# Kernel tuning notes

Hardware: AMD Instinct MI355X
Metric: run time of the kernel (lower is better)

## Reference

```python
import jax, jax.numpy as jnp
import numpy as np

B, L, D, H = 1, 4096, 512, 8
HD = D // H  # head_dim = 64


def _relative_bias(rel, length):
    # rel: [H, 2L] learnable; returns [H, L, L] relative position bias
    h = rel.shape[0]
    r = jnp.tile(rel, (1, length))                      # [H, 2L*L]
    r = r[:, : length * (2 * length - 1)]
    r = r.reshape(h, length, 2 * length - 1)
    return r[..., length - 1:]                          # [H, L, L]


def setup_inputs() -> dict:
    key = jax.random.key(0)
    ks = jax.random.split(key, 12)
    std = D ** -0.5
    inp = {
        "x": jax.random.normal(ks[0], (B, L, D), jnp.float32),
        "pos_embed": jax.random.normal(ks[1], (L, D), jnp.float32) * std,
        "rel_bias": jnp.zeros((H, 2 * L), jnp.float32) + 0.01 * jax.random.normal(ks[2], (H, 2 * L), jnp.float32),
        "Wq": jax.random.normal(ks[3], (D, H, HD), jnp.float32) * std,
        "bq": jnp.zeros((H, HD), jnp.float32),
        "Wk": jax.random.normal(ks[4], (D, H, HD), jnp.float32) * std,
        "bk": jnp.zeros((H, HD), jnp.float32),
        "Wv": jax.random.normal(ks[5], (D, H, HD), jnp.float32) * std,
        "bv": jnp.zeros((H, HD), jnp.float32),
        "Wo": jax.random.normal(ks[6], (H, HD, D), jnp.float32) * (D ** -0.5),
        "bo": jnp.zeros((D,), jnp.float32),
    }
    return inp


def reference(x, pos_embed, rel_bias, Wq, bq, Wk, bk, Wv, bv, Wo, bo):
    # Positional embedding
    x = x + pos_embed
    # QKV projections: [B, L, H, HD]
    q = jnp.einsum("bld,dhk->blhk", x, Wq) + bq
    k = jnp.einsum("bld,dhk->blhk", x, Wk) + bk
    v = jnp.einsum("bld,dhk->blhk", x, Wv) + bv
    # Scaled dot-product attention with relative attention bias
    depth = q.shape[-1]
    q = q / jnp.sqrt(jnp.asarray(depth, q.dtype))
    scores = jnp.einsum("bqhd,bkhd->bhqk", q, k)       # [B, H, L, L]
    bias = _relative_bias(rel_bias, x.shape[1])         # [H, L, L]
    scores = scores + bias[None]
    attn = jax.nn.softmax(scores, axis=-1)
    out = jnp.einsum("bhqk,bkhd->bqhd", attn, v)       # [B, L, H, HD]
    # Output projection back to D
    return jnp.einsum("bqhd,hdD->bqD", out, Wo) + bo
```

## Files before the change

### kernel.cpp

```cpp
#include <hip/hip_runtime.h>
#include <hip/hip_bf16.h>


typedef __attribute__((ext_vector_type(8))) short bf16x8;
typedef __attribute__((ext_vector_type(4))) short bf16x4;
typedef __attribute__((ext_vector_type(4))) float f32x4;
typedef __attribute__((ext_vector_type(2))) unsigned u32x2;

#define QSCALE (0.125f * 1.4426950408889634f)

__device__ __forceinline__ short f2bf(float f) {
    unsigned u = __builtin_bit_cast(unsigned, f);
    u += 0x7fff + ((u >> 16) & 1);
    return (short)(u >> 16);
}

__device__ __forceinline__ f32x4 mfma32(bf16x8 a, bf16x8 b, f32x4 c) {
    return __builtin_amdgcn_mfma_f32_16x16x32_bf16(a, b, c, 0, 0, 0);
}

__device__ __forceinline__ unsigned cvtpk(float a, float b) {
    unsigned r;
    asm("v_cvt_pk_bf16_f32 %0, %1, %2" : "=v"(r) : "v"(a), "v"(b));
    return r;
}

__global__ __launch_bounds__(256) void k_prep_xp(const float* __restrict__ x,
                                                 const float* __restrict__ pos,
                                                 short* __restrict__ xp) {
    int i = (blockIdx.x * 256 + threadIdx.x) * 8;
    float4 a0 = *(const float4*)(x + i);
    float4 a1 = *(const float4*)(x + i + 4);
    float4 b0 = *(const float4*)(pos + i);
    float4 b1 = *(const float4*)(pos + i + 4);
    bf16x8 v;
    v[0] = f2bf(a0.x + b0.x); v[1] = f2bf(a0.y + b0.y);
    v[2] = f2bf(a0.z + b0.z); v[3] = f2bf(a0.w + b0.w);
    v[4] = f2bf(a1.x + b1.x); v[5] = f2bf(a1.y + b1.y);
    v[6] = f2bf(a1.z + b1.z); v[7] = f2bf(a1.w + b1.w);
    *(bf16x8*)(xp + i) = v;
}

__global__ __launch_bounds__(256) void k_prep_wqkv(const float* __restrict__ Wq,
                                                   const float* __restrict__ Wk,
                                                   const float* __restrict__ Wv,
                                                   short* __restrict__ WT) {
    int idx = blockIdx.x * 256 + threadIdx.x;
    int n = idx >> 9, k = idx & 511;
    int nn = n & 511;
    const float* src = (n < 512) ? Wq : (n < 1024 ? Wk : Wv);
    float scale = (n < 512) ? QSCALE : 1.0f;
    WT[idx] = f2bf(src[k * 512 + nn] * scale);
}

__global__ __launch_bounds__(256) void k_prep_wo(const float* __restrict__ Wo,
                                                 short* __restrict__ WoT) {
    int idx = blockIdx.x * 256 + threadIdx.x;
    int n = idx >> 9, k = idx & 511;
    WoT[idx] = f2bf(Wo[k * 512 + n]);
}

__global__ __launch_bounds__(256) void k_prep_rel2(const float* __restrict__ rel,
                                                   float* __restrict__ rel2) {
    int i = blockIdx.x * 256 + threadIdx.x;
    rel2[i] = rel[i] * 1.4426950408889634f;
}

__global__ __launch_bounds__(256) void k_vt(const short* __restrict__ Vg,
                                            short* __restrict__ VT) {
    __shared__ short tile[64][72];
    const int tid = threadIdx.x;
    const int h = blockIdx.y, kvb = blockIdx.x * 64;
    const short* src = Vg + (size_t)h * 4096 * 64;
    short* dst = VT + (size_t)h * 64 * 4096;
    #pragma unroll
    for (int i = 0; i < 2; ++i) {
        int ch = tid + 256 * i;
        int r = ch >> 3, c = (ch & 7) * 8;
        *(uint4*)&tile[r][c] = *(const uint4*)(src + (size_t)(kvb + r) * 64 + c);
    }
    __syncthreads();
    #pragma unroll
    for (int i = 0; i < 2; ++i) {
        int ch = tid + 256 * i;
        int d = ch >> 3, kc = (ch & 7) * 8;
        bf16x8 v;
        #pragma unroll
        for (int j = 0; j < 8; ++j) v[j] = tile[kc + j][d];
        *(bf16x8*)(dst + (size_t)d * 4096 + kvb + kc) = v;
    }
}

template <int MODE>
__global__ __launch_bounds__(256) void k_gemm(const short* __restrict__ A,
                                              const short* __restrict__ Bt,
                                              const float* __restrict__ bias0,
                                              const float* __restrict__ bias1,
                                              const float* __restrict__ bias2,
                                              short* __restrict__ Qg,
                                              short* __restrict__ Kg,
                                              short* __restrict__ Vg,
                                              float* __restrict__ Cout) {
    __shared__ short Al[128][72];
    __shared__ short Bl[128][72];
    const int tid = threadIdx.x;
    const int lane = tid & 63, wid = tid >> 6;
    const int wm = wid >> 1, wn = wid & 1;
    const int mb = blockIdx.y * 128, nb = blockIdx.x * 128;
    const int lr = lane & 15, lg = lane >> 4;

    f32x4 acc[4][4] = {};

    for (int kk = 0; kk < 512; kk += 64) {
        #pragma unroll
        for (int i = 0; i < 4; ++i) {
            int o = tid + 256 * i;
            int row = o >> 3, c8 = (o & 7) * 8;
            *(uint4*)(&Al[row][c8]) = *(const uint4*)(A + (size_t)(mb + row) * 512 + kk + c8);
            *(uint4*)(&Bl[row][c8]) = *(const uint4*)(Bt + (size_t)(nb + row) * 512 + kk + c8);
        }
        __syncthreads();
        #pragma unroll
        for (int ks = 0; ks < 2; ++ks) {
            bf16x8 af[4], bfr[4];
            #pragma unroll
            for (int t = 0; t < 4; ++t) {
                af[t]  = *(const bf16x8*)(&Al[wm * 64 + t * 16 + lr][ks * 32 + lg * 8]);
                bfr[t] = *(const bf16x8*)(&Bl[wn * 64 + t * 16 + lr][ks * 32 + lg * 8]);
            }
            #pragma unroll
            for (int mt = 0; mt < 4; ++mt)
                #pragma unroll
                for (int nt = 0; nt < 4; ++nt)
                    acc[mt][nt] = mfma32(af[mt], bfr[nt], acc[mt][nt]);
        }
        __syncthreads();
    }

    #pragma unroll
    for (int mt = 0; mt < 4; ++mt) {
        #pragma unroll
        for (int nt = 0; nt < 4; ++nt) {
            #pragma unroll
            for (int r = 0; r < 4; ++r) {
                int m = mb + wm * 64 + mt * 16 + lg * 4 + r;
                int n = nb + wn * 64 + nt * 16 + lr;
                float v = acc[mt][nt][r];
                if (MODE == 0) {
                    int which = n >> 9;
                    int nn = n & 511;
                    int hh = nn >> 6, hd = nn & 63;
                    const float* bp = (which == 0) ? bias0 : (which == 1 ? bias1 : bias2);
                    v += bp[nn] * (which == 0 ? QSCALE : 1.0f);
                    short* dst = (which == 0) ? Qg : (which == 1 ? Kg : Vg);
                    dst[((size_t)hh * 4096 + m) * 64 + hd] = f2bf(v);
                } else {
                    Cout[(size_t)m * 512 + n] = v + bias0[n];
                }
            }
        }
    }
}

__global__ __launch_bounds__(256, 2) void k_attn3(const short* __restrict__ Qg,
                                                  const short* __restrict__ Kg,
                                                  const short* __restrict__ VT,
                                                  const float* __restrict__ rel2,
                                                  short* __restrict__ AO) {
    __shared__ __align__(16) char smem[70656];

    const int tid = threadIdx.x;
    const int lane = tid & 63, sp = tid >> 6;
    const int lr = lane & 15, lg = lane >> 4;
    const int bid = blockIdx.x;
    const int h = bid & 7;
    const int qb = (bid >> 3) * 64;

    short* Pw = (short*)smem + sp * 1152;

    const short* Qh = Qg + (size_t)h * 4096 * 64;
    const short* Kh = Kg + (size_t)h * 4096 * 64;
    const short* VTh = VT + (size_t)h * 64 * 4096;

    bf16x8 qf[4][2];
    #pragma unroll
    for (int qt = 0; qt < 4; ++qt)
        #pragma unroll
        for (int dk = 0; dk < 2; ++dk)
            qf[qt][dk] = *(const bf16x8*)(Qh + (size_t)(qb + qt * 16 + lr) * 64 + dk * 32 + lg * 8);

    const int kvbase = sp * 1024;
    const short* kp = Kh + (size_t)kvbase * 64;
    const short* vp = VTh + kvbase;
    const float* bp = rel2 + h * 8192 + (kvbase + 4095 - qb) + lg * 4 - lr;

    f32x4 acc[4][4] = {};
    f32x4 lacc[4] = {};

    bf16x8 ones;
    #pragma unroll
    for (int i = 0; i < 8; ++i) ones[i] = (short)0x3F80;

    #pragma unroll 1
    for (int it = 0; it < 16; ++it) {
        bf16x8 kf[4][2];
        #pragma unroll
        for (int t = 0; t < 4; ++t) {
            kf[t][0] = *(const bf16x8*)(kp + (size_t)(t * 16 + lr) * 64 + lg * 8);
            kf[t][1] = *(const bf16x8*)(kp + (size_t)(t * 16 + lr) * 64 + 32 + lg * 8);
        }
        bf16x8 vf[4][2];
        #pragma unroll
        for (int dt = 0; dt < 4; ++dt)
            #pragma unroll
            for (int w = 0; w < 2; ++w)
                vf[dt][w] = *(const bf16x8*)(vp + (size_t)(dt * 16 + lr) * 4096 + w * 32 + lg * 8);

        #pragma unroll
        for (int qt = 0; qt < 4; ++qt) {
            f32x4 cin[4];
            #pragma unroll
            for (int t = 0; t < 4; ++t)
                #pragma unroll
                for (int r = 0; r < 4; ++r)
                    cin[t][r] = bp[(t - qt) * 16 + r];

            unsigned pk0[4], pk1[4];
            #pragma unroll
            for (int t = 0; t < 4; ++t) {
                f32x4 z = mfma32(kf[t][0], qf[qt][0], cin[t]);
                z = mfma32(kf[t][1], qf[qt][1], z);
                float p0 = exp2f(z[0]), p1 = exp2f(z[1]);
                float p2 = exp2f(z[2]), p3 = exp2f(z[3]);
                pk0[t] = cvtpk(p0, p1);
                pk1[t] = cvtpk(p2, p3);
            }

            asm volatile("s_waitcnt lgkmcnt(0)" ::: "memory");
            __builtin_amdgcn_sched_barrier(0);
            #pragma unroll
            for (int t = 0; t < 4; ++t) {
                u32x2 pk;
                pk[0] = pk0[t]; pk[1] = pk1[t];
                *(u32x2*)(Pw + lr * 72 + t * 16 + lg * 4) = pk;
            }
            __builtin_amdgcn_sched_barrier(0);

            bf16x8 pb0 = *(const bf16x8*)(Pw + lr * 72 + lg * 8);
            bf16x8 pb1 = *(const bf16x8*)(Pw + lr * 72 + 32 + lg * 8);

            lacc[qt] = mfma32(ones, pb0, lacc[qt]);
            lacc[qt] = mfma32(ones, pb1, lacc[qt]);

            #pragma unroll
            for (int dt = 0; dt < 4; ++dt) {
                acc[qt][dt] = mfma32(vf[dt][0], pb0, acc[qt][dt]);
                acc[qt][dt] = mfma32(vf[dt][1], pb1, acc[qt][dt]);
            }
        }
        kp += 64 * 64;
        vp += 64;
        bp += 64;
    }

    __builtin_amdgcn_sched_barrier(0);
    __syncthreads();
    __builtin_amdgcn_sched_barrier(0);

    float* Opart = (float*)smem;
    float* Lpart = (float*)(smem + 69632);
    #pragma unroll
    for (int qt = 0; qt < 4; ++qt) {
        #pragma unroll
        for (int dt = 0; dt < 4; ++dt)
            *(f32x4*)&Opart[((sp * 4 + qt) * 16 + lr) * 68 + dt * 16 + lg * 4] = acc[qt][dt];
        if (lg == 0) Lpart[(sp * 4 + qt) * 16 + lr] = lacc[qt][0];
    }
    __builtin_amdgcn_sched_barrier(0);
    __syncthreads();
    __builtin_amdgcn_sched_barrier(0);
    {
        const int qi = tid >> 2, quad = tid & 3;
        const int qt2 = qi >> 4, qr = qi & 15;
        f32x4 s0 = {}, s1 = {}, s2 = {}, s3 = {};
        float lt = 0.f;
        #pragma unroll
        for (int s = 0; s < 4; ++s) {
            const float* o = &Opart[((s * 4 + qt2) * 16 + qr) * 68 + quad * 16];
            s0 += *(const f32x4*)(o + 0);
            s1 += *(const f32x4*)(o + 4);
            s2 += *(const f32x4*)(o + 8);
            s3 += *(const f32x4*)(o + 12);
            lt += Lpart[(s * 4 + qt2) * 16 + qr];
        }
        float inv = 1.0f / lt;
        bf16x8 o0, o1;
        o0[0] = f2bf(s0[0] * inv); o0[1] = f2bf(s0[1] * inv);
        o0[2] = f2bf(s0[2] * inv); o0[3] = f2bf(s0[3] * inv);
        o0[4] = f2bf(s1[0] * inv); o0[5] = f2bf(s1[1] * inv);
        o0[6] = f2bf(s1[2] * inv); o0[7] = f2bf(s1[3] * inv);
        o1[0] = f2bf(s2[0] * inv); o1[1] = f2bf(s2[1] * inv);
        o1[2] = f2bf(s2[2] * inv); o1[3] = f2bf(s2[3] * inv);
        o1[4] = f2bf(s3[0] * inv); o1[5] = f2bf(s3[1] * inv);
        o1[6] = f2bf(s3[2] * inv); o1[7] = f2bf(s3[3] * inv);
        short* dst = AO + (size_t)(qb + qi) * 512 + h * 64 + quad * 16;
        *(bf16x8*)(dst) = o0;
        *(bf16x8*)(dst + 8) = o1;
    }
}

extern "C" void kernel_launch(void* const* d_in, const int* in_sizes, int n_in,
                              void* d_out, int out_size, void* d_ws, size_t ws_size,
                              hipStream_t stream) {
    const float* x   = (const float*)d_in[0];
    const float* pos = (const float*)d_in[1];
    const float* rel = (const float*)d_in[2];
    const float* Wq  = (const float*)d_in[3];
    const float* bq  = (const float*)d_in[4];
    const float* Wk  = (const float*)d_in[5];
    const float* bk  = (const float*)d_in[6];
    const float* Wv  = (const float*)d_in[7];
    const float* bv  = (const float*)d_in[8];
    const float* Wo  = (const float*)d_in[9];
    const float* bo  = (const float*)d_in[10];
    float* out = (float*)d_out;

    char* ws = (char*)d_ws;
    short* xp    = (short*)ws;  ws += (size_t)4096 * 512 * 2;
    short* WqkvT = (short*)ws;  ws += (size_t)1536 * 512 * 2;
    short* WoT   = (short*)ws;  ws += (size_t)512 * 512 * 2;
    short* Qg    = (short*)ws;  ws += (size_t)8 * 4096 * 64 * 2;
    short* Kg    = (short*)ws;  ws += (size_t)8 * 4096 * 64 * 2;
    short* Vg    = (short*)ws;  ws += (size_t)8 * 4096 * 64 * 2;
    short* AO    = (short*)ws;  ws += (size_t)4096 * 512 * 2;
    float* rel2  = (float*)ws;  ws += (size_t)8 * 8192 * 4;
    short* VT    = xp;

    k_prep_xp<<<dim3(4096 * 512 / (256 * 8)), 256, 0, stream>>>(x, pos, xp);
    k_prep_wqkv<<<dim3(1536 * 512 / 256), 256, 0, stream>>>(Wq, Wk, Wv, WqkvT);
    k_prep_wo<<<dim3(512 * 512 / 256), 256, 0, stream>>>(Wo, WoT);
    k_prep_rel2<<<dim3(8 * 8192 / 256), 256, 0, stream>>>(rel, rel2);

    k_gemm<0><<<dim3(12, 32), 256, 0, stream>>>(xp, WqkvT, bq, bk, bv, Qg, Kg, Vg, nullptr);
    k_vt<<<dim3(64, 8), 256, 0, stream>>>(Vg, VT);
    k_attn3<<<dim3(512), 256, 0, stream>>>(Qg, Kg, VT, rel2, AO);
    k_gemm<1><<<dim3(4, 32), 256, 0, stream>>>(AO, WoT, bo, nullptr, nullptr,
                                               nullptr, nullptr, nullptr, out);
}
```

Before: 130.0 us.

## Split attention KV range across blocks and merge partials in separate kernel

The attention kernel changes from one block per 64 queries, with four waves splitting the KV range and reducing in shared memory, to blocks whose four waves each own 32 queries of a 128-query tile while the block handles one quarter of the KV range. Partial outputs and row sums go to global workspace, and a new merge kernel sums the four partials, normalises and writes bf16. The aim is to cut LDS use and registers so four blocks fit per CU, doubling the grid for occupancy. The cost is extra global traffic for fp32 partials (about 32MB written and read) plus another kernel launch.

After: 330.1 us. +153.9%, slower.

```diff
diff --git a/kernel.cpp b/kernel.cpp
--- a/kernel.cpp
+++ b/kernel.cpp
@@ -162,40 +162,42 @@
     }
 }
 
-__global__ __launch_bounds__(256, 2) void k_attn3(const short* __restrict__ Qg,
+__global__ __launch_bounds__(256, 4) void k_attn4(const short* __restrict__ Qg,
                                                   const short* __restrict__ Kg,
                                                   const short* __restrict__ VT,
                                                   const float* __restrict__ rel2,
-                                                  short* __restrict__ AO) {
-    __shared__ __align__(16) char smem[70656];
+                                                  float* __restrict__ Opar,
+                                                  float* __restrict__ Lpar) {
+    __shared__ __align__(16) char smem[9216];
 
     const int tid = threadIdx.x;
-    const int lane = tid & 63, sp = tid >> 6;
+    const int lane = tid & 63, wv = tid >> 6;
     const int lr = lane & 15, lg = lane >> 4;
     const int bid = blockIdx.x;
     const int h = bid & 7;
-    const int qb = (bid >> 3) * 64;
-
-    short* Pw = (short*)smem + sp * 1152;
+    const int s = (bid >> 3) & 3;
+    const int qb = (bid >> 5) * 128 + wv * 32;
+
+    short* Pw = (short*)smem + wv * 1152;
 
     const short* Qh = Qg + (size_t)h * 4096 * 64;
     const short* Kh = Kg + (size_t)h * 4096 * 64;
     const short* VTh = VT + (size_t)h * 64 * 4096;
 
-    bf16x8 qf[4][2];
-    #pragma unroll
-    for (int qt = 0; qt < 4; ++qt)
+    bf16x8 qf[2][2];
+    #pragma unroll
+    for (int qt = 0; qt < 2; ++qt)
         #pragma unroll
         for (int dk = 0; dk < 2; ++dk)
             qf[qt][dk] = *(const bf16x8*)(Qh + (size_t)(qb + qt * 16 + lr) * 64 + dk * 32 + lg * 8);
 
-    const int kvbase = sp * 1024;
+    const int kvbase = s * 1024;
     const short* kp = Kh + (size_t)kvbase * 64;
     const short* vp = VTh + kvbase;
     const float* bp = rel2 + h * 8192 + (kvbase + 4095 - qb) + lg * 4 - lr;
 
-    f32x4 acc[4][4] = {};
-    f32x4 lacc[4] = {};
+    f32x4 acc[2][4] = {};
+    f32x4 lacc[2] = {};
 
     bf16x8 ones;
     #pragma unroll
@@ -217,7 +219,7 @@
                 vf[dt][w] = *(const bf16x8*)(vp + (size_t)(dt * 16 + lr) * 4096 + w * 32 + lg * 8);
 
         #pragma unroll
-        for (int qt = 0; qt < 4; ++qt) {
+        for (int qt = 0; qt < 2; ++qt) {
             f32x4 cin[4];
             #pragma unroll
             for (int t = 0; t < 4; ++t)
@@ -263,50 +265,35 @@
         bp += 64;
     }
 
-    __builtin_amdgcn_sched_barrier(0);
-    __syncthreads();
-    __builtin_amdgcn_sched_barrier(0);
-
-    float* Opart = (float*)smem;
-    float* Lpart = (float*)(smem + 69632);
-    #pragma unroll
-    for (int qt = 0; qt < 4; ++qt) {
+    const size_t base = (size_t)(s * 8 + h) * 4096 + qb;
+    #pragma unroll
+    for (int qt = 0; qt < 2; ++qt) {
         #pragma unroll
         for (int dt = 0; dt < 4; ++dt)
-            *(f32x4*)&Opart[((sp * 4 + qt) * 16 + lr) * 68 + dt * 16 + lg * 4] = acc[qt][dt];
-        if (lg == 0) Lpart[(sp * 4 + qt) * 16 + lr] = lacc[qt][0];
-    }
-    __builtin_amdgcn_sched_barrier(0);
-    __syncthreads();
-    __builtin_amdgcn_sched_barrier(0);
-    {
-        const int qi = tid >> 2, quad = tid & 3;
-        const int qt2 = qi >> 4, qr = qi & 15;
-        f32x4 s0 = {}, s1 = {}, s2 = {}, s3 = {};
-        float lt = 0.f;
-        #pragma unroll
-        for (int s = 0; s < 4; ++s) {
-            const float* o = &Opart[((s * 4 + qt2) * 16 + qr) * 68 + quad * 16];
-            s0 += *(const f32x4*)(o + 0);
-            s1 += *(const f32x4*)(o + 4);
-            s2 += *(const f32x4*)(o + 8);
-            s3 += *(const f32x4*)(o + 12);
-            lt += Lpart[(s * 4 + qt2) * 16 + qr];
-        }
-        float inv = 1.0f / lt;
-        bf16x8 o0, o1;
-        o0[0] = f2bf(s0[0] * inv); o0[1] = f2bf(s0[1] * inv);
-        o0[2] = f2bf(s0[2] * inv); o0[3] = f2bf(s0[3] * inv);
-        o0[4] = f2bf(s1[0] * inv); o0[5] = f2bf(s1[1] * inv);
-        o0[6] = f2bf(s1[2] * inv); o0[7] = f2bf(s1[3] * inv);
-        o1[0] = f2bf(s2[0] * inv); o1[1] = f2bf(s2[1] * inv);
-        o1[2] = f2bf(s2[2] * inv); o1[3] = f2bf(s2[3] * inv);
-        o1[4] = f2bf(s3[0] * inv); o1[5] = f2bf(s3[1] * inv);
-        o1[6] = f2bf(s3[2] * inv); o1[7] = f2bf(s3[3] * inv);
-        short* dst = AO + (size_t)(qb + qi) * 512 + h * 64 + quad * 16;
-        *(bf16x8*)(dst) = o0;
-        *(bf16x8*)(dst + 8) = o1;
-    }
+            *(f32x4*)(Opar + (base + qt * 16 + lr) * 64 + dt * 16 + lg * 4) = acc[qt][dt];
+        if (lg == 0) Lpar[base + qt * 16 + lr] = lacc[qt][0];
+    }
+}
+
+__global__ __launch_bounds__(256) void k_merge(const float* __restrict__ Opar,
+                                               const float* __restrict__ Lpar,
+                                               short* __restrict__ AO) {
+    int idx = blockIdx.x * 256 + threadIdx.x;
+    int dq = idx & 15;
+    int q = (idx >> 4) & 4095;
+    int h = idx >> 16;
+    f32x4 sacc = {};
+    float lt = 0.f;
+    #pragma unroll
+    for (int s = 0; s < 4; ++s) {
+        sacc += *(const f32x4*)(Opar + ((size_t)(s * 8 + h) * 4096 + q) * 64 + dq * 4);
+        lt += Lpar[(size_t)(s * 8 + h) * 4096 + q];
+    }
+    float inv = 1.0f / lt;
+    bf16x4 o;
+    o[0] = f2bf(sacc[0] * inv); o[1] = f2bf(sacc[1] * inv);
+    o[2] = f2bf(sacc[2] * inv); o[3] = f2bf(sacc[3] * inv);
+    *(bf16x4*)(AO + (size_t)q * 512 + h * 64 + dq * 4) = o;
 }
 
 extern "C" void kernel_launch(void* const* d_in, const int* in_sizes, int n_in,
@@ -334,6 +321,8 @@
     short* Vg    = (short*)ws;  ws += (size_t)8 * 4096 * 64 * 2;
     short* AO    = (short*)ws;  ws += (size_t)4096 * 512 * 2;
     float* rel2  = (float*)ws;  ws += (size_t)8 * 8192 * 4;
+    float* Opar  = (float*)ws;  ws += (size_t)4 * 8 * 4096 * 64 * 4;
+    float* Lpar  = (float*)ws;  ws += (size_t)4 * 8 * 4096 * 4;
     short* VT    = xp;
 
     k_prep_xp<<<dim3(4096 * 512 / (256 * 8)), 256, 0, stream>>>(x, pos, xp);
@@ -343,7 +332,8 @@
 
     k_gemm<0><<<dim3(12, 32), 256, 0, stream>>>(xp, WqkvT, bq, bk, bv, Qg, Kg, Vg, nullptr);
     k_vt<<<dim3(64, 8), 256, 0, stream>>>(Vg, VT);
-    k_attn3<<<dim3(512), 256, 0, stream>>>(Qg, Kg, VT, rel2, AO);
+    k_attn4<<<dim3(1024), 256, 0, stream>>>(Qg, Kg, VT, rel2, Opar, Lpar);
+    k_merge<<<dim3(2048), 256, 0, stream>>>(Opar, Lpar, AO);
     k_gemm<1><<<dim3(4, 32), 256, 0, stream>>>(AO, WoT, bo, nullptr, nullptr,
                                                nullptr, nullptr, nullptr, out);
 }
```
